# Performance work log

Hardware: AMD Instinct MI355X
Metric: run time of the kernel (lower is better)

## Reference

```python
import jax, jax.numpy as jnp
import numpy as np

T, B, D = 2048, 1, 1024
N_HEAD, D_HEAD, D_FF = 16, 64, 4096
LN_EPS = 1e-5


def layer_norm(x, g, b):
    m = jnp.mean(x, axis=-1, keepdims=True)
    v = jnp.mean(jnp.square(x - m), axis=-1, keepdims=True)
    return (x - m) * jax.lax.rsqrt(v + LN_EPS) * g + b


def rel_shift(x):
    # x: (qlen, klen, bsz, n_head) -> Transformer-XL relative shift
    q, k, b, h = x.shape
    zp = jnp.zeros((q, 1, b, h), dtype=x.dtype)
    x = jnp.concatenate([zp, x], axis=1)            # (q, k+1, b, h)
    x = x.reshape(k + 1, q, b, h)[1:].reshape(q, k, b, h)
    return x


def setup_inputs() -> dict:
    key = jax.random.key(0)
    ks = jax.random.split(key, 12)
    s = lambda fan: 1.0 / np.sqrt(fan)
    inp = {
        "input": jax.random.normal(ks[0], (T, B, D), jnp.float32),
        "pos": jax.random.normal(ks[1], (T, 1, D), jnp.float32),
        "r_w_bias": jax.random.normal(ks[2], (N_HEAD, D_HEAD), jnp.float32) * 0.02,
        "r_r_bias": jax.random.normal(ks[3], (N_HEAD, D_HEAD), jnp.float32) * 0.02,
        # causal mask: True = masked (future positions)
        "mask": jnp.triu(jnp.ones((T, T), dtype=bool), k=1),
        "ln1_g": jnp.ones((D,), jnp.float32),
        "ln1_b": jnp.zeros((D,), jnp.float32),
        "qkv_w": jax.random.normal(ks[4], (D, 3 * D), jnp.float32) * s(D),
        "r_w": jax.random.normal(ks[5], (D, D), jnp.float32) * s(D),
        "o_w": jax.random.normal(ks[6], (D, D), jnp.float32) * s(D),
        "ln2_g": jnp.ones((D,), jnp.float32),
        "ln2_b": jnp.zeros((D,), jnp.float32),
        "ff_w1": jax.random.normal(ks[7], (D, D_FF), jnp.float32) * s(D),
        "ff_b1": jnp.zeros((D_FF,), jnp.float32),
        "ff_w2": jax.random.normal(ks[8], (D_FF, D), jnp.float32) * s(D_FF),
        "ff_b2": jnp.zeros((D,), jnp.float32),
    }
    return inp


def reference(input, pos, r_w_bias, r_r_bias, mask, ln1_g, ln1_b, qkv_w, r_w,
              o_w, ln2_g, ln2_b, ff_w1, ff_b1, ff_w2, ff_b2):
    scale = 1.0 / np.sqrt(D_HEAD)
    # preprocess_attn: layernorm
    q_in = layer_norm(input, ln1_g, ln1_b)                      # (T,B,D)
    w_heads = jnp.einsum('tbd,de->tbe', q_in, qkv_w)            # (T,B,3D)
    w_q, w_k, w_v = jnp.split(w_heads, 3, axis=-1)
    w_q = w_q.reshape(T, B, N_HEAD, D_HEAD)
    w_k = w_k.reshape(T, B, N_HEAD, D_HEAD)
    w_v = w_v.reshape(T, B, N_HEAD, D_HEAD)
    r_k = (pos[:, 0] @ r_w).reshape(T, N_HEAD, D_HEAD)          # (T,h,dh)

    AC = jnp.einsum('ibnd,jbnd->ijbn', w_q + r_w_bias, w_k)     # (T,T,B,h)
    BD = rel_shift(jnp.einsum('ibnd,jnd->ijbn', w_q + r_r_bias, r_k))
    score = (AC + BD) * scale
    score = jnp.where(mask[:, :, None, None], jnp.finfo(score.dtype).min, score)
    probs = jax.nn.softmax(score, axis=1)                       # coverage
    attn_vec = jnp.einsum('ijbn,jbnd->ibnd', probs, w_v).reshape(T, B, D)
    attn_out = jnp.einsum('tbd,de->tbe', attn_vec, o_w)
    # postprocess_attn: (dropout=identity) + residual
    x = input + attn_out
    # FFN block: layernorm > linear-relu-linear > residual
    y = layer_norm(x, ln2_g, ln2_b)
    y = jax.nn.relu(jnp.einsum('tbd,df->tbf', y, ff_w1) + ff_b1)
    y = jnp.einsum('tbf,fd->tbd', y, ff_w2) + ff_b2
    x = x + y
    return x, probs
```

## Files before the change

### kernel.cpp

```cpp
#include <hip/hip_runtime.h>
#include <hip/hip_bf16.h>
#include <stdint.h>

using bf16 = __hip_bfloat16;
using short8 = __attribute__((ext_vector_type(8))) short;
using f32x4 = __attribute__((ext_vector_type(4))) float;

#define T_SEQ 2048
#define DMODEL 1024
#define NHEAD 16
#define DHEAD 64
#define DFF 4096

struct __align__(8) bf16x4 { bf16 x, y, z, w; };

__device__ __forceinline__ void async_cp16(const bf16* g, bf16* l) {
  __builtin_amdgcn_global_load_lds(
      (const __attribute__((address_space(1))) uint32_t*)g,
      (__attribute__((address_space(3))) uint32_t*)l, 16, 0, 0);
}

__global__ __launch_bounds__(256) void transpose_cvt(const float* __restrict__ src,
                                                     bf16* __restrict__ dst,
                                                     int R, int C) {
  __shared__ float tile[32][33];
  int bx = blockIdx.x * 32;
  int by = blockIdx.y * 32;
  int tx = threadIdx.x, ty = threadIdx.y;
#pragma unroll
  for (int r = 0; r < 32; r += 8)
    tile[ty + r][tx] = src[(long)(by + ty + r) * C + bx + tx];
  __syncthreads();
#pragma unroll
  for (int r = 0; r < 32; r += 8)
    dst[(long)(bx + ty + r) * R + by + tx] = __float2bfloat16(tile[tx][ty + r]);
}

__global__ __launch_bounds__(256) void cvt_bf16(const float* __restrict__ src,
                                                bf16* __restrict__ dst, int n4) {
  int idx = blockIdx.x * 256 + threadIdx.x;
  if (idx < n4) {
    float4 v = ((const float4*)src)[idx];
    bf16x4 o{__float2bfloat16(v.x), __float2bfloat16(v.y),
             __float2bfloat16(v.z), __float2bfloat16(v.w)};
    ((bf16x4*)dst)[idx] = o;
  }
}

__global__ __launch_bounds__(256) void ln_cvt(const float* __restrict__ x,
                                              const float* __restrict__ g,
                                              const float* __restrict__ b,
                                              bf16* __restrict__ out) {
  int row = blockIdx.x;
  int tid = threadIdx.x;
  float4 v = ((const float4*)(x + (long)row * DMODEL))[tid];
  float s = v.x + v.y + v.z + v.w;
  float s2 = v.x * v.x + v.y * v.y + v.z * v.z + v.w * v.w;
#pragma unroll
  for (int off = 32; off > 0; off >>= 1) {
    s += __shfl_down(s, off);
    s2 += __shfl_down(s2, off);
  }
  __shared__ float ss[4], ss2[4];
  int wave = tid >> 6, lane = tid & 63;
  if (lane == 0) { ss[wave] = s; ss2[wave] = s2; }
  __syncthreads();
  s = ss[0] + ss[1] + ss[2] + ss[3];
  s2 = ss2[0] + ss2[1] + ss2[2] + ss2[3];
  float mean = s * (1.0f / DMODEL);
  float var = s2 * (1.0f / DMODEL) - mean * mean;
  float rstd = rsqrtf(var + 1e-5f);
  float4 gg = ((const float4*)g)[tid];
  float4 bb = ((const float4*)b)[tid];
  bf16x4 o{__float2bfloat16((v.x - mean) * rstd * gg.x + bb.x),
           __float2bfloat16((v.y - mean) * rstd * gg.y + bb.y),
           __float2bfloat16((v.z - mean) * rstd * gg.z + bb.z),
           __float2bfloat16((v.w - mean) * rstd * gg.w + bb.w)};
  ((bf16x4*)(out + (long)row * DMODEL))[tid] = o;
}

template <int BN, class Epi>
__global__ __launch_bounds__(256) void gemm_bt(const bf16* __restrict__ A,
                                               const bf16* __restrict__ Bt,
                                               int M, int N, int K,
                                               long aZstride, long bZstride, Epi epi) {
  constexpr int BM = 128;
  constexpr int BK = 32;
  constexpr int NT = BN / 32;
  __shared__ bf16 As[BM * BK];
  __shared__ bf16 Bs[BN * BK];

  const int bm = blockIdx.y, bn = blockIdx.x, z = blockIdx.z;
  const bf16* Ab = A + (long)z * aZstride;
  const bf16* Bb = Bt + (long)z * bZstride;

  const int tid = threadIdx.x;
  const int lane = tid & 63;
  const int wave = tid >> 6;
  const int wr = wave >> 1;
  const int wc = wave & 1;
  const int kEnd = epi.kmax(bm, bn, K);

  const f32x4 zero4 = {0.f, 0.f, 0.f, 0.f};
  f32x4 acc[4][NT];
#pragma unroll
  for (int mt = 0; mt < 4; ++mt)
#pragma unroll
    for (int nt = 0; nt < NT; ++nt) acc[mt][nt] = zero4;

  const int sr = tid >> 2;
  const int sc = (tid & 3) * 8;
  const bf16* aG0 = Ab + (long)(bm * BM + sr) * K + sc;
  const bf16* aG1 = Ab + (long)(bm * BM + 64 + sr) * K + sc;
  bf16* aL0 = As + tid * 8;
  bf16* aL1 = As + 2048 + tid * 8;
  const bf16* bG0 = Bb + (long)(bn * BN + sr) * K + sc;
  bf16* bL0 = Bs + tid * 8;
  const bf16* bG1 = Bb + (long)(bn * BN + 64 + sr) * K + sc;
  bf16* bL1 = Bs + 2048 + tid * 8;

  const int aRow = wr * 64 + (lane & 15);
  const int bRow = wc * (BN / 2) + (lane & 15);
  const int kq = (lane >> 4) * 8;

  for (int k0 = 0; k0 < kEnd; k0 += BK) {
    __syncthreads();
    async_cp16(aG0, aL0);
    async_cp16(aG1, aL1);
    async_cp16(bG0, bL0);
    if constexpr (BN == 128) async_cp16(bG1, bL1);
    aG0 += BK; aG1 += BK; bG0 += BK;
    if constexpr (BN == 128) bG1 += BK;
    __syncthreads();
    short8 af[4], bfr[NT];
#pragma unroll
    for (int mt = 0; mt < 4; ++mt)
      af[mt] = *(const short8*)(As + (aRow + mt * 16) * BK + kq);
#pragma unroll
    for (int nt = 0; nt < NT; ++nt)
      bfr[nt] = *(const short8*)(Bs + (bRow + nt * 16) * BK + kq);
#pragma unroll
    for (int mt = 0; mt < 4; ++mt)
#pragma unroll
      for (int nt = 0; nt < NT; ++nt)
        acc[mt][nt] = __builtin_amdgcn_mfma_f32_16x16x32_bf16(af[mt], bfr[nt],
                                                              acc[mt][nt], 0, 0, 0);
  }

  const int rBase = (lane >> 4) * 4;
  const int cOff = lane & 15;
#pragma unroll
  for (int mt = 0; mt < 4; ++mt) {
#pragma unroll
    for (int nt = 0; nt < NT; ++nt) {
      int row = bm * BM + wr * 64 + mt * 16 + rBase;
      int col = bn * BN + wc * (BN / 2) + nt * 16 + cOff;
      f32x4 v = acc[mt][nt];
#pragma unroll
      for (int r = 0; r < 4; ++r) epi.store(z, row + r, col, v[r]);
    }
  }
}

struct EpiQKV {
  bf16 *Qh, *Kb, *Vt;
  __device__ int kmax(int, int, int K) const { return K; }
  __device__ void store(int, int row, int col, float v) const {
    int n = (col >> 6) & 15, d = col & 63;
    long hoff = ((long)n * T_SEQ + row) * DHEAD + d;
    if (col < DMODEL) {
      Qh[hoff] = __float2bfloat16(v);
    } else if (col < 2 * DMODEL) {
      Kb[hoff] = __float2bfloat16(v);
    } else {
      Vt[((long)n * DHEAD + d) * T_SEQ + row] = __float2bfloat16(v);
    }
  }
};

struct EpiRk {
  bf16* Rk;
  __device__ int kmax(int, int, int K) const { return K; }
  __device__ void store(int, int row, int col, float v) const {
    int n = col >> 6, d = col & 63;
    Rk[((long)n * T_SEQ + row) * DHEAD + d] = __float2bfloat16(v);
  }
};

struct EpiPV {
  bf16* av;
  __device__ int kmax(int bm, int, int K) const {
    int kl = (bm + 1) * 128;
    return kl < K ? kl : K;
  }
  __device__ void store(int z, int row, int col, float v) const {
    av[(long)row * DMODEL + z * DHEAD + col] = __float2bfloat16(v);
  }
};

struct EpiO {
  float* xws;
  const float* inp;
  __device__ int kmax(int, int, int K) const { return K; }
  __device__ void store(int, int row, int col, float v) const {
    long idx = (long)row * DMODEL + col;
    xws[idx] = v + inp[idx];
  }
};

struct EpiFF1 {
  bf16* h;
  const float* b1;
  __device__ int kmax(int, int, int K) const { return K; }
  __device__ void store(int, int row, int col, float v) const {
    h[(long)row * DFF + col] = __float2bfloat16(fmaxf(v + b1[col], 0.f));
  }
};

struct EpiFF2 {
  float* out;
  const float* b2;
  const float* xws;
  __device__ int kmax(int, int, int K) const { return K; }
  __device__ void store(int, int row, int col, float v) const {
    long idx = (long)row * DMODEL + col;
    out[idx] = v + b2[col] + xws[idx];
  }
};

__global__ __launch_bounds__(256) void bias_k(const bf16* __restrict__ Kb,
                                              const bf16* __restrict__ Rk,
                                              const float* __restrict__ rwb,
                                              const float* __restrict__ rrb,
                                              float* __restrict__ acB,
                                              float* __restrict__ rrbR) {
  int idx = blockIdx.x * 256 + threadIdx.x;
  int n = idx >> 11;
  const short8* kp = (const short8*)(Kb + (long)idx * DHEAD);
  const short8* rp = (const short8*)(Rk + (long)idx * DHEAD);
  float s1 = 0.f, s2 = 0.f;
#pragma unroll
  for (int q8 = 0; q8 < 8; ++q8) {
    short8 kv = kp[q8], rv = rp[q8];
#pragma unroll
    for (int e = 0; e < 8; ++e) {
      float w1 = rwb[n * DHEAD + q8 * 8 + e];
      float w2 = rrb[n * DHEAD + q8 * 8 + e];
      s1 += w1 * __bfloat162float(((const bf16*)&kv)[e]);
      s2 += w2 * __bfloat162float(((const bf16*)&rv)[e]);
    }
  }
  acB[idx] = s1;
  rrbR[idx] = s2;
}

__global__ __launch_bounds__(256) void score_k(const bf16* __restrict__ Qh,
                                               const bf16* __restrict__ Kb,
                                               const bf16* __restrict__ Rk,
                                               const float* __restrict__ acB,
                                               const float* __restrict__ rrbR,
                                               bf16* __restrict__ score) {
  const int bn = blockIdx.x, bm = blockIdx.y, z = blockIdx.z;
  if (bn > bm) return;
  __shared__ char smem[70656];
  bf16* Qs  = (bf16*)smem;
  bf16* Ks  = (bf16*)(smem + 16384);
  bf16* Bnd = (bf16*)(smem + 32768);

  const int tid = threadIdx.x;
  const int lane = tid & 63, wave = tid >> 6;
  const int wr = wave >> 1, wc = wave & 1;
  const int kq = (lane >> 4) * 8;
  const int l15 = lane & 15;
  const int base = 128 * (bn - bm) + T_SEQ - 1 - 128;

  const bf16* Qg = Qh + ((long)z * T_SEQ + bm * 128) * DHEAD;
  const bf16* Kg = Kb + ((long)z * T_SEQ + bn * 128) * DHEAD;
  const bf16* Rg = Rk + (long)z * T_SEQ * DHEAD;

#pragma unroll
  for (int it = 0; it < 4; ++it) {
    int s = it * 256 + tid;
    int kh = s >> 9, r = (s >> 2) & 127, c = (s & 3) * 8;
    async_cp16(Qg + (long)r * DHEAD + kh * 32 + c, Qs + s * 8);
    async_cp16(Kg + (long)r * DHEAD + kh * 32 + c, Ks + s * 8);
  }
#pragma unroll
  for (int it = 0; it < 8; ++it) {
    int s = it * 256 + tid;
    int kh = s >> 10, u = (s >> 2) & 255, c = (s & 3) * 8;
    int g = base + u;
    g = g < 0 ? 0 : (g > T_SEQ - 1 ? T_SEQ - 1 : g);
    async_cp16(Rg + (long)g * DHEAD + kh * 32 + c, Bnd + s * 8);
  }

  const f32x4 zero4 = {0.f, 0.f, 0.f, 0.f};
  f32x4 accA[4][4], accW[4][8];
#pragma unroll
  for (int mt = 0; mt < 4; ++mt) {
#pragma unroll
    for (int nt = 0; nt < 4; ++nt) accA[mt][nt] = zero4;
#pragma unroll
    for (int ut = 0; ut < 8; ++ut) accW[mt][ut] = zero4;
  }

  __syncthreads();
#pragma unroll
  for (int kh = 0; kh < 2; ++kh) {
    short8 qa[4], kf[4], wf[8];
#pragma unroll
    for (int mt = 0; mt < 4; ++mt)
      qa[mt] = *(const short8*)(Qs + kh * 4096 + (wr * 64 + mt * 16 + l15) * 32 + kq);
#pragma unroll
    for (int nt = 0; nt < 4; ++nt)
      kf[nt] = *(const short8*)(Ks + kh * 4096 + (wc * 64 + nt * 16 + l15) * 32 + kq);
#pragma unroll
    for (int ut = 0; ut < 8; ++ut)
      wf[ut] = *(const short8*)(Bnd + kh * 8192 + (wc * 128 + ut * 16 + l15) * 32 + kq);
#pragma unroll
    for (int mt = 0; mt < 4; ++mt) {
#pragma unroll
      for (int nt = 0; nt < 4; ++nt)
        accA[mt][nt] = __builtin_amdgcn_mfma_f32_16x16x32_bf16(qa[mt], kf[nt], accA[mt][nt], 0, 0, 0);
#pragma unroll
      for (int ut = 0; ut < 8; ++ut)
        accW[mt][ut] = __builtin_amdgcn_mfma_f32_16x16x32_bf16(qa[mt], wf[ut], accW[mt][ut], 0, 0, 0);
    }
  }

  float wbias[8];
#pragma unroll
  for (int ut = 0; ut < 8; ++ut) {
    int u = wc * 128 + ut * 16 + l15;
    int g = base + u;
    g = g < 0 ? 0 : (g > T_SEQ - 1 ? T_SEQ - 1 : g);
    wbias[ut] = rrbR[(long)z * T_SEQ + g];
  }
  float abias[4];
#pragma unroll
  for (int nt = 0; nt < 4; ++nt)
    abias[nt] = acB[(long)z * T_SEQ + bn * 128 + wc * 64 + nt * 16 + l15];

  __syncthreads();

  bf16* Wl = (bf16*)smem + wr * (64 * 276);
  const int quad4 = (lane >> 4) * 4;
  const int umin = wr ? 1 : 65;
  const int umax = wr ? 191 : 255;
#pragma unroll
  for (int mt = 0; mt < 4; ++mt) {
#pragma unroll
    for (int ut = 0; ut < 8; ++ut) {
      int ub = wc * 128 + ut * 16;
      if (ub + 15 < umin || ub > umax) continue;
      int lr = mt * 16 + quad4;
      int u = ub + l15;
#pragma unroll
      for (int reg = 0; reg < 4; ++reg)
        Wl[(lr + reg) * 276 + u] = __float2bfloat16(accW[mt][ut][reg] + wbias[ut]);
    }
  }
  __syncthreads();

  bf16* srow = score + (long)z * T_SEQ * T_SEQ;
#pragma unroll
  for (int mt = 0; mt < 4; ++mt) {
#pragma unroll
    for (int nt = 0; nt < 4; ++nt) {
      int lr = mt * 16 + quad4;
      int c = wc * 64 + nt * 16 + l15;
#pragma unroll
      for (int reg = 0; reg < 4; ++reg) {
        int rl = lr + reg;
        int r = wr * 64 + rl;
        int u = c - r + 128;
        float v = accA[mt][nt][reg] + abias[nt] +
                  __bfloat162float(Wl[rl * 276 + u]);
        srow[(long)(bm * 128 + r) * T_SEQ + bn * 128 + c] = __float2bfloat16(v);
      }
    }
  }
}

__global__ __launch_bounds__(1024) void softmax_k(const bf16* __restrict__ S,
                                                  float* __restrict__ probs,
                                                  bf16* __restrict__ pb) {
  constexpr int HS = T_SEQ + 8;
  __shared__ bf16 pl[NHEAD * HS];
  __shared__ float rinv_s[NHEAD];
  const int i = blockIdx.x;
  const int tid = threadIdx.x;
  const int h = tid >> 6, lane = tid & 63;
  const float scale = 0.125f;
  const int nch = (i >> 9) + 1;

  const bf16* row = S + (long)h * T_SEQ * T_SEQ + (long)i * T_SEQ;

  short8 v[4];
  float m = -1e30f;
#pragma unroll
  for (int c = 0; c < 4; ++c) {
    if (c < nch) {
      int j0 = c * 512 + lane * 8;
      v[c] = *(const short8*)(row + j0);
#pragma unroll
      for (int e = 0; e < 8; ++e) {
        float s = (j0 + e <= i) ? __bfloat162float(((const bf16*)&v[c])[e]) * scale : -1e30f;
        m = fmaxf(m, s);
      }
    }
  }
#pragma unroll
  for (int off = 1; off < 64; off <<= 1) m = fmaxf(m, __shfl_xor(m, off));

  float l = 0.f;
#pragma unroll
  for (int c = 0; c < 4; ++c) {
    if (c < nch) {
      int j0 = c * 512 + lane * 8;
      short8 o;
#pragma unroll
      for (int e = 0; e < 8; ++e) {
        float p = 0.f;
        if (j0 + e <= i) {
          p = __expf(__bfloat162float(((const bf16*)&v[c])[e]) * scale - m);
          l += p;
        }
        ((bf16*)&o)[e] = __float2bfloat16(p);
      }
      *(short8*)(pl + h * HS + j0) = o;
    }
  }
#pragma unroll
  for (int off = 1; off < 64; off <<= 1) l += __shfl_xor(l, off);
  if (lane == 0) rinv_s[h] = 1.f / l;
  __syncthreads();

  float* prow = probs + (long)i * T_SEQ * NHEAD;
  const int n0 = (tid & 3) * 4;
  const float rv0 = rinv_s[n0 + 0], rv1 = rinv_s[n0 + 1];
  const float rv2 = rinv_s[n0 + 2], rv3 = rinv_s[n0 + 3];
#pragma unroll
  for (int it = 0; it < 8; ++it) {
    int o = it * 1024 + tid;
    int j = o >> 2;
    float4 f = {0.f, 0.f, 0.f, 0.f};
    if (j <= i) {
      f.x = __bfloat162float(pl[(n0 + 0) * HS + j]) * rv0;
      f.y = __bfloat162float(pl[(n0 + 1) * HS + j]) * rv1;
      f.z = __bfloat162float(pl[(n0 + 2) * HS + j]) * rv2;
      f.w = __bfloat162float(pl[(n0 + 3) * HS + j]) * rv3;
    }
    ((float4*)prow)[o] = f;
  }

  const int kround = ((i >> 7) + 1) << 7;
  bf16* prow_b = pb + (long)h * T_SEQ * T_SEQ + (long)i * T_SEQ;
  const float rinv = rinv_s[h];
  for (int j0 = lane * 8; j0 < kround; j0 += 512) {
    short8 pv = *(const short8*)(pl + h * HS + j0);
    short8 o;
#pragma unroll
    for (int e = 0; e < 8; ++e)
      ((bf16*)&o)[e] = __float2bfloat16(__bfloat162float(((const bf16*)&pv)[e]) * rinv);
    *(short8*)(prow_b + j0) = o;
  }
}

extern "C" void kernel_launch(void* const* d_in, const int* in_sizes, int n_in,
                              void* d_out, int out_size, void* d_ws, size_t ws_size,
                              hipStream_t stream) {
  const float* input = (const float*)d_in[0];
  const float* pos   = (const float*)d_in[1];
  const float* rwb   = (const float*)d_in[2];
  const float* rrb   = (const float*)d_in[3];
  const float* ln1g  = (const float*)d_in[5];
  const float* ln1b  = (const float*)d_in[6];
  const float* qkvw  = (const float*)d_in[7];
  const float* rw    = (const float*)d_in[8];
  const float* ow    = (const float*)d_in[9];
  const float* ln2g  = (const float*)d_in[10];
  const float* ln2b  = (const float*)d_in[11];
  const float* ffw1  = (const float*)d_in[12];
  const float* ffb1  = (const float*)d_in[13];
  const float* ffw2  = (const float*)d_in[14];
  const float* ffb2  = (const float*)d_in[15];
  float* out = (float*)d_out;

  size_t off = 0;
  auto alloc = [&](size_t bytes) -> char* {
    char* p = (char*)d_ws + off;
    off += (bytes + 255) & ~(size_t)255;
    return p;
  };
  bf16* wqkvT = (bf16*)alloc(3072L * 1024 * 2);
  bf16* wrT   = (bf16*)alloc(1024L * 1024 * 2);
  bf16* woT   = (bf16*)alloc(1024L * 1024 * 2);
  bf16* wf1T  = (bf16*)alloc(4096L * 1024 * 2);
  bf16* wf2T  = (bf16*)alloc(1024L * 4096 * 2);
  bf16* qin   = (bf16*)alloc(2048L * 1024 * 2);
  bf16* posb  = (bf16*)alloc(2048L * 1024 * 2);
  bf16* Qh    = (bf16*)alloc(16L * 2048 * 64 * 2);
  bf16* Kb    = (bf16*)alloc(16L * 2048 * 64 * 2);
  bf16* Vt    = (bf16*)alloc(16L * 64 * 2048 * 2);
  bf16* Rk    = (bf16*)alloc(16L * 2048 * 64 * 2);
  float* acB  = (float*)alloc(16L * 2048 * 4);
  float* rrbR = (float*)alloc(16L * 2048 * 4);
  bf16* ACb   = (bf16*)alloc(16L * 2048 * 2048 * 2);
  bf16* pb    = (bf16*)alloc(16L * 2048 * 2048 * 2);
  bf16* av    = (bf16*)alloc(2048L * 1024 * 2);
  float* xws  = (float*)alloc(2048L * 1024 * 4);
  bf16* yb    = (bf16*)alloc(2048L * 1024 * 2);
  bf16* hb    = (bf16*)alloc(2048L * 4096 * 2);

  dim3 tb(32, 8);
  transpose_cvt<<<dim3(3072 / 32, 1024 / 32), tb, 0, stream>>>(qkvw, wqkvT, 1024, 3072);
  transpose_cvt<<<dim3(1024 / 32, 1024 / 32), tb, 0, stream>>>(rw, wrT, 1024, 1024);
  transpose_cvt<<<dim3(1024 / 32, 1024 / 32), tb, 0, stream>>>(ow, woT, 1024, 1024);
  transpose_cvt<<<dim3(4096 / 32, 1024 / 32), tb, 0, stream>>>(ffw1, wf1T, 1024, 4096);
  transpose_cvt<<<dim3(1024 / 32, 4096 / 32), tb, 0, stream>>>(ffw2, wf2T, 4096, 1024);
  cvt_bf16<<<2048, 256, 0, stream>>>(pos, posb, 2048 * 1024 / 4);
  ln_cvt<<<2048, 256, 0, stream>>>(input, ln1g, ln1b, qin);

  {
    EpiQKV e{Qh, Kb, Vt};
    gemm_bt<128, EpiQKV><<<dim3(24, 16, 1), 256, 0, stream>>>(qin, wqkvT, 2048, 3072, 1024, 0, 0, e);
  }
  {
    EpiRk e{Rk};
    gemm_bt<64, EpiRk><<<dim3(16, 16, 1), 256, 0, stream>>>(posb, wrT, 2048, 1024, 1024, 0, 0, e);
  }
  bias_k<<<128, 256, 0, stream>>>(Kb, Rk, rwb, rrb, acB, rrbR);
  score_k<<<dim3(16, 16, 16), 256, 0, stream>>>(Qh, Kb, Rk, acB, rrbR, ACb);
  softmax_k<<<2048, 1024, 0, stream>>>(ACb, out + 2048L * 1024, pb);
  {
    EpiPV e{av};
    gemm_bt<64, EpiPV><<<dim3(1, 16, 16), 256, 0, stream>>>(pb, Vt, 2048, 64, 2048,
                                                            2048L * 2048, 64L * 2048, e);
  }
  {
    EpiO e{xws, input};
    gemm_bt<64, EpiO><<<dim3(16, 16, 1), 256, 0, stream>>>(av, woT, 2048, 1024, 1024, 0, 0, e);
  }
  ln_cvt<<<2048, 256, 0, stream>>>(xws, ln2g, ln2b, yb);
  {
    EpiFF1 e{hb, ffb1};
    gemm_bt<128, EpiFF1><<<dim3(32, 16, 1), 256, 0, stream>>>(yb, wf1T, 2048, 4096, 1024, 0, 0, e);
  }
  {
    EpiFF2 e{out, ffb2, xws};
    gemm_bt<64, EpiFF2><<<dim3(16, 16, 1), 256, 0, stream>>>(hb, wf2T, 2048, 1024, 4096, 0, 0, e);
  }
}
```

Before: 790.1 us.

## Merge weight-conversion launches, skip masked MFMAs, stage score tile for coalesced stores

Folds the five weight transpose-and-convert launches and the pos conversion into a single launch that picks its matrix from the block index. In the score kernel, it skips MFMAs for AC tiles fully above the diagonal on diagonal blocks, and for positional-band tiles that are never read. The score tile is also staged through shared memory so it can be written with 16-byte coalesced stores instead of scattered 2-byte stores. This adds an extra barrier and LDS round-trip, and upper-triangle values on diagonal blocks now hold only bias terms, which the softmax presumably masks.

```diff
diff --git a/kernel.cpp b/kernel.cpp
--- a/kernel.cpp
+++ b/kernel.cpp
@@ -20,13 +20,33 @@
       (__attribute__((address_space(3))) uint32_t*)l, 16, 0, 0);
 }
 
-__global__ __launch_bounds__(256) void transpose_cvt(const float* __restrict__ src,
-                                                     bf16* __restrict__ dst,
-                                                     int R, int C) {
+__global__ __launch_bounds__(256) void transpose_all(
+    const float* __restrict__ s0, bf16* __restrict__ d0,
+    const float* __restrict__ s1, bf16* __restrict__ d1,
+    const float* __restrict__ s2, bf16* __restrict__ d2,
+    const float* __restrict__ s3, bf16* __restrict__ d3,
+    const float* __restrict__ s4, bf16* __restrict__ d4,
+    const float* __restrict__ s5, bf16* __restrict__ d5) {
   __shared__ float tile[32][33];
-  int bx = blockIdx.x * 32;
-  int by = blockIdx.y * 32;
+  int b = blockIdx.x;
   int tx = threadIdx.x, ty = threadIdx.y;
+  if (b >= 13312) {
+    int idx = (b - 13312) * 256 + ty * 32 + tx;
+    float4 v = ((const float4*)s5)[idx];
+    bf16x4 o{__float2bfloat16(v.x), __float2bfloat16(v.y),
+             __float2bfloat16(v.z), __float2bfloat16(v.w)};
+    ((bf16x4*)d5)[idx] = o;
+    return;
+  }
+  const float* src; bf16* dst; int R, C, t;
+  if (b < 3072)      { src = s0; dst = d0; R = 1024; C = 3072; t = b; }
+  else if (b < 4096) { src = s1; dst = d1; R = 1024; C = 1024; t = b - 3072; }
+  else if (b < 5120) { src = s2; dst = d2; R = 1024; C = 1024; t = b - 4096; }
+  else if (b < 9216) { src = s3; dst = d3; R = 1024; C = 4096; t = b - 5120; }
+  else               { src = s4; dst = d4; R = 4096; C = 1024; t = b - 9216; }
+  int tcols = C >> 5;
+  int bx = (t % tcols) * 32;
+  int by = (t / tcols) * 32;
 #pragma unroll
   for (int r = 0; r < 32; r += 8)
     tile[ty + r][tx] = src[(long)(by + ty + r) * C + bx + tx];
@@ -34,17 +54,6 @@
 #pragma unroll
   for (int r = 0; r < 32; r += 8)
     dst[(long)(bx + ty + r) * R + by + tx] = __float2bfloat16(tile[tx][ty + r]);
-}
-
-__global__ __launch_bounds__(256) void cvt_bf16(const float* __restrict__ src,
-                                                bf16* __restrict__ dst, int n4) {
-  int idx = blockIdx.x * 256 + threadIdx.x;
-  if (idx < n4) {
-    float4 v = ((const float4*)src)[idx];
-    bf16x4 o{__float2bfloat16(v.x), __float2bfloat16(v.y),
-             __float2bfloat16(v.z), __float2bfloat16(v.w)};
-    ((bf16x4*)dst)[idx] = o;
-  }
 }
 
 __global__ __launch_bounds__(256) void ln_cvt(const float* __restrict__ x,
@@ -294,6 +303,23 @@
     async_cp16(Rg + (long)g * DHEAD + kh * 32 + c, Bnd + s * 8);
   }
 
+  int ubs[8];
+  bool keepP[4][8];
+  bool needUt[8];
+#pragma unroll
+  for (int ut = 0; ut < 8; ++ut) { ubs[ut] = (ut * 2 + wc) * 16; needUt[ut] = false; }
+#pragma unroll
+  for (int mt = 0; mt < 4; ++mt) {
+    int r0 = wr * 64 + mt * 16;
+#pragma unroll
+    for (int ut = 0; ut < 8; ++ut) {
+      bool k = (ubs[ut] + 15 >= 113 - r0) && (ubs[ut] <= 255 - r0);
+      keepP[mt][ut] = k;
+      needUt[ut] = needUt[ut] || k;
+    }
+  }
+  const bool diag = (bm == bn);
+
   const f32x4 zero4 = {0.f, 0.f, 0.f, 0.f};
   f32x4 accA[4][4], accW[4][8];
 #pragma unroll
@@ -316,23 +342,25 @@
       kf[nt] = *(const short8*)(Ks + kh * 4096 + (wc * 64 + nt * 16 + l15) * 32 + kq);
 #pragma unroll
     for (int ut = 0; ut < 8; ++ut)
-      wf[ut] = *(const short8*)(Bnd + kh * 8192 + (wc * 128 + ut * 16 + l15) * 32 + kq);
+      if (needUt[ut])
+        wf[ut] = *(const short8*)(Bnd + kh * 8192 + (ubs[ut] + l15) * 32 + kq);
 #pragma unroll
     for (int mt = 0; mt < 4; ++mt) {
 #pragma unroll
       for (int nt = 0; nt < 4; ++nt)
-        accA[mt][nt] = __builtin_amdgcn_mfma_f32_16x16x32_bf16(qa[mt], kf[nt], accA[mt][nt], 0, 0, 0);
+        if (!(diag && (wc * 64 + nt * 16 > wr * 64 + mt * 16 + 15)))
+          accA[mt][nt] = __builtin_amdgcn_mfma_f32_16x16x32_bf16(qa[mt], kf[nt], accA[mt][nt], 0, 0, 0);
 #pragma unroll
       for (int ut = 0; ut < 8; ++ut)
-        accW[mt][ut] = __builtin_amdgcn_mfma_f32_16x16x32_bf16(qa[mt], wf[ut], accW[mt][ut], 0, 0, 0);
+        if (keepP[mt][ut])
+          accW[mt][ut] = __builtin_amdgcn_mfma_f32_16x16x32_bf16(qa[mt], wf[ut], accW[mt][ut], 0, 0, 0);
     }
   }
 
   float wbias[8];
 #pragma unroll
   for (int ut = 0; ut < 8; ++ut) {
-    int u = wc * 128 + ut * 16 + l15;
-    int g = base + u;
+    int g = base + ubs[ut] + l15;
     g = g < 0 ? 0 : (g > T_SEQ - 1 ? T_SEQ - 1 : g);
     wbias[ut] = rrbR[(long)z * T_SEQ + g];
   }
@@ -345,16 +373,13 @@
 
   bf16* Wl = (bf16*)smem + wr * (64 * 276);
   const int quad4 = (lane >> 4) * 4;
-  const int umin = wr ? 1 : 65;
-  const int umax = wr ? 191 : 255;
 #pragma unroll
   for (int mt = 0; mt < 4; ++mt) {
 #pragma unroll
     for (int ut = 0; ut < 8; ++ut) {
-      int ub = wc * 128 + ut * 16;
-      if (ub + 15 < umin || ub > umax) continue;
+      if (!keepP[mt][ut]) continue;
       int lr = mt * 16 + quad4;
-      int u = ub + l15;
+      int u = ubs[ut] + l15;
 #pragma unroll
       for (int reg = 0; reg < 4; ++reg)
         Wl[(lr + reg) * 276 + u] = __float2bfloat16(accW[mt][ut][reg] + wbias[ut]);
@@ -362,7 +387,6 @@
   }
   __syncthreads();
 
-  bf16* srow = score + (long)z * T_SEQ * T_SEQ;
 #pragma unroll
   for (int mt = 0; mt < 4; ++mt) {
 #pragma unroll
@@ -372,13 +396,34 @@
 #pragma unroll
       for (int reg = 0; reg < 4; ++reg) {
         int rl = lr + reg;
-        int r = wr * 64 + rl;
-        int u = c - r + 128;
-        float v = accA[mt][nt][reg] + abias[nt] +
-                  __bfloat162float(Wl[rl * 276 + u]);
-        srow[(long)(bm * 128 + r) * T_SEQ + bn * 128 + c] = __float2bfloat16(v);
+        int u = c - (wr * 64 + rl) + 128;
+        accA[mt][nt][reg] += abias[nt] + __bfloat162float(Wl[rl * 276 + u]);
       }
     }
+  }
+  __syncthreads();
+
+  bf16* Ss = (bf16*)smem;
+#pragma unroll
+  for (int mt = 0; mt < 4; ++mt) {
+#pragma unroll
+    for (int nt = 0; nt < 4; ++nt) {
+      int lr = mt * 16 + quad4;
+      int c = wc * 64 + nt * 16 + l15;
+#pragma unroll
+      for (int reg = 0; reg < 4; ++reg)
+        Ss[(wr * 64 + lr + reg) * 132 + c] = __float2bfloat16(accA[mt][nt][reg]);
+    }
+  }
+  __syncthreads();
+
+  bf16* srow = score + (long)z * T_SEQ * T_SEQ;
+#pragma unroll
+  for (int it = 0; it < 8; ++it) {
+    int s = it * 256 + tid;
+    int row = s >> 4, c8 = (s & 15) * 8;
+    *(short8*)(srow + (long)(bm * 128 + row) * T_SEQ + bn * 128 + c8) =
+        *(const short8*)(Ss + row * 132 + c8);
   }
 }
 
@@ -514,12 +559,8 @@
   bf16* hb    = (bf16*)alloc(2048L * 4096 * 2);
 
   dim3 tb(32, 8);
-  transpose_cvt<<<dim3(3072 / 32, 1024 / 32), tb, 0, stream>>>(qkvw, wqkvT, 1024, 3072);
-  transpose_cvt<<<dim3(1024 / 32, 1024 / 32), tb, 0, stream>>>(rw, wrT, 1024, 1024);
-  transpose_cvt<<<dim3(1024 / 32, 1024 / 32), tb, 0, stream>>>(ow, woT, 1024, 1024);
-  transpose_cvt<<<dim3(4096 / 32, 1024 / 32), tb, 0, stream>>>(ffw1, wf1T, 1024, 4096);
-  transpose_cvt<<<dim3(1024 / 32, 4096 / 32), tb, 0, stream>>>(ffw2, wf2T, 4096, 1024);
-  cvt_bf16<<<2048, 256, 0, stream>>>(pos, posb, 2048 * 1024 / 4);
+  transpose_all<<<15360, tb, 0, stream>>>(qkvw, wqkvT, rw, wrT, ow, woT,
+                                          ffw1, wf1T, ffw2, wf2T, pos, posb);
   ln_cvt<<<2048, 256, 0, stream>>>(input, ln1g, ln1b, qin);
 
   {
```

Measured after the change: 824.6 us. 4.4% more time.

## Merge weight conversions, shrink GEMM tiles, split-K FF2 with atomics

Applied to the files above, without the earlier changes.

Merges the five weight transposes and the pos conversion into one kernel launch. Adds a BM template parameter so the Rk, PV and O GEMMs use 64x64 tiles, doubling their block counts to fill more CUs. FF2 is split four ways along K and accumulates with atomic adds into an output pre-initialised with residual plus bias, which gives more parallelism. The trade-off is extra atomic traffic, non-deterministic summation order and one added init pass.

```diff
diff --git a/kernel.cpp b/kernel.cpp
--- a/kernel.cpp
+++ b/kernel.cpp
@@ -20,13 +20,33 @@
       (__attribute__((address_space(3))) uint32_t*)l, 16, 0, 0);
 }
 
-__global__ __launch_bounds__(256) void transpose_cvt(const float* __restrict__ src,
-                                                     bf16* __restrict__ dst,
-                                                     int R, int C) {
+__global__ __launch_bounds__(256) void transpose_all(
+    const float* __restrict__ s0, bf16* __restrict__ d0,
+    const float* __restrict__ s1, bf16* __restrict__ d1,
+    const float* __restrict__ s2, bf16* __restrict__ d2,
+    const float* __restrict__ s3, bf16* __restrict__ d3,
+    const float* __restrict__ s4, bf16* __restrict__ d4,
+    const float* __restrict__ s5, bf16* __restrict__ d5) {
   __shared__ float tile[32][33];
-  int bx = blockIdx.x * 32;
-  int by = blockIdx.y * 32;
+  int b = blockIdx.x;
   int tx = threadIdx.x, ty = threadIdx.y;
+  if (b >= 13312) {
+    int idx = (b - 13312) * 256 + ty * 32 + tx;
+    float4 v = ((const float4*)s5)[idx];
+    bf16x4 o{__float2bfloat16(v.x), __float2bfloat16(v.y),
+             __float2bfloat16(v.z), __float2bfloat16(v.w)};
+    ((bf16x4*)d5)[idx] = o;
+    return;
+  }
+  const float* src; bf16* dst; int R, C, t;
+  if (b < 3072)      { src = s0; dst = d0; R = 1024; C = 3072; t = b; }
+  else if (b < 4096) { src = s1; dst = d1; R = 1024; C = 1024; t = b - 3072; }
+  else if (b < 5120) { src = s2; dst = d2; R = 1024; C = 1024; t = b - 4096; }
+  else if (b < 9216) { src = s3; dst = d3; R = 1024; C = 4096; t = b - 5120; }
+  else               { src = s4; dst = d4; R = 4096; C = 1024; t = b - 9216; }
+  int tcols = C >> 5;
+  int bx = (t % tcols) * 32;
+  int by = (t / tcols) * 32;
 #pragma unroll
   for (int r = 0; r < 32; r += 8)
     tile[ty + r][tx] = src[(long)(by + ty + r) * C + bx + tx];
@@ -34,17 +54,6 @@
 #pragma unroll
   for (int r = 0; r < 32; r += 8)
     dst[(long)(bx + ty + r) * R + by + tx] = __float2bfloat16(tile[tx][ty + r]);
-}
-
-__global__ __launch_bounds__(256) void cvt_bf16(const float* __restrict__ src,
-                                                bf16* __restrict__ dst, int n4) {
-  int idx = blockIdx.x * 256 + threadIdx.x;
-  if (idx < n4) {
-    float4 v = ((const float4*)src)[idx];
-    bf16x4 o{__float2bfloat16(v.x), __float2bfloat16(v.y),
-             __float2bfloat16(v.z), __float2bfloat16(v.w)};
-    ((bf16x4*)dst)[idx] = o;
-  }
 }
 
 __global__ __launch_bounds__(256) void ln_cvt(const float* __restrict__ x,
@@ -79,13 +88,23 @@
   ((bf16x4*)(out + (long)row * DMODEL))[tid] = o;
 }
 
-template <int BN, class Epi>
+__global__ __launch_bounds__(256) void ff2_init(const float* __restrict__ xws,
+                                                const float* __restrict__ b2,
+                                                float* __restrict__ out) {
+  int idx = blockIdx.x * 256 + threadIdx.x;
+  float4 x = ((const float4*)xws)[idx];
+  float4 b = ((const float4*)b2)[idx & 255];
+  float4 o{x.x + b.x, x.y + b.y, x.z + b.z, x.w + b.w};
+  ((float4*)out)[idx] = o;
+}
+
+template <int BM, int BN, class Epi>
 __global__ __launch_bounds__(256) void gemm_bt(const bf16* __restrict__ A,
                                                const bf16* __restrict__ Bt,
                                                int M, int N, int K,
                                                long aZstride, long bZstride, Epi epi) {
-  constexpr int BM = 128;
   constexpr int BK = 32;
+  constexpr int MT = BM / 32;
   constexpr int NT = BN / 32;
   __shared__ bf16 As[BM * BK];
   __shared__ bf16 Bs[BN * BK];
@@ -99,48 +118,50 @@
   const int wave = tid >> 6;
   const int wr = wave >> 1;
   const int wc = wave & 1;
-  const int kEnd = epi.kmax(bm, bn, K);
+  const int kBeg = epi.kmin(bm, bn, z);
+  const int kEnd = epi.kmax(bm, bn, z, K);
 
   const f32x4 zero4 = {0.f, 0.f, 0.f, 0.f};
-  f32x4 acc[4][NT];
-#pragma unroll
-  for (int mt = 0; mt < 4; ++mt)
+  f32x4 acc[MT][NT];
+#pragma unroll
+  for (int mt = 0; mt < MT; ++mt)
 #pragma unroll
     for (int nt = 0; nt < NT; ++nt) acc[mt][nt] = zero4;
 
   const int sr = tid >> 2;
   const int sc = (tid & 3) * 8;
-  const bf16* aG0 = Ab + (long)(bm * BM + sr) * K + sc;
-  const bf16* aG1 = Ab + (long)(bm * BM + 64 + sr) * K + sc;
+  const bf16* aG0 = Ab + (long)(bm * BM + sr) * K + kBeg + sc;
+  const bf16* aG1 = Ab + (long)(bm * BM + 64 + sr) * K + kBeg + sc;
   bf16* aL0 = As + tid * 8;
   bf16* aL1 = As + 2048 + tid * 8;
-  const bf16* bG0 = Bb + (long)(bn * BN + sr) * K + sc;
+  const bf16* bG0 = Bb + (long)(bn * BN + sr) * K + kBeg + sc;
   bf16* bL0 = Bs + tid * 8;
-  const bf16* bG1 = Bb + (long)(bn * BN + 64 + sr) * K + sc;
+  const bf16* bG1 = Bb + (long)(bn * BN + 64 + sr) * K + kBeg + sc;
   bf16* bL1 = Bs + 2048 + tid * 8;
 
-  const int aRow = wr * 64 + (lane & 15);
+  const int aRow = wr * (BM / 2) + (lane & 15);
   const int bRow = wc * (BN / 2) + (lane & 15);
   const int kq = (lane >> 4) * 8;
 
-  for (int k0 = 0; k0 < kEnd; k0 += BK) {
+  for (int k0 = kBeg; k0 < kEnd; k0 += BK) {
     __syncthreads();
     async_cp16(aG0, aL0);
-    async_cp16(aG1, aL1);
+    if constexpr (BM == 128) async_cp16(aG1, aL1);
     async_cp16(bG0, bL0);
     if constexpr (BN == 128) async_cp16(bG1, bL1);
-    aG0 += BK; aG1 += BK; bG0 += BK;
+    aG0 += BK; bG0 += BK;
+    if constexpr (BM == 128) aG1 += BK;
     if constexpr (BN == 128) bG1 += BK;
     __syncthreads();
-    short8 af[4], bfr[NT];
-#pragma unroll
-    for (int mt = 0; mt < 4; ++mt)
+    short8 af[MT], bfr[NT];
+#pragma unroll
+    for (int mt = 0; mt < MT; ++mt)
       af[mt] = *(const short8*)(As + (aRow + mt * 16) * BK + kq);
 #pragma unroll
     for (int nt = 0; nt < NT; ++nt)
       bfr[nt] = *(const short8*)(Bs + (bRow + nt * 16) * BK + kq);
 #pragma unroll
-    for (int mt = 0; mt < 4; ++mt)
+    for (int mt = 0; mt < MT; ++mt)
 #pragma unroll
       for (int nt = 0; nt < NT; ++nt)
         acc[mt][nt] = __builtin_amdgcn_mfma_f32_16x16x32_bf16(af[mt], bfr[nt],
@@ -150,10 +171,10 @@
   const int rBase = (lane >> 4) * 4;
   const int cOff = lane & 15;
 #pragma unroll
-  for (int mt = 0; mt < 4; ++mt) {
+  for (int mt = 0; mt < MT; ++mt) {
 #pragma unroll
     for (int nt = 0; nt < NT; ++nt) {
-      int row = bm * BM + wr * 64 + mt * 16 + rBase;
+      int row = bm * BM + wr * (BM / 2) + mt * 16 + rBase;
       int col = bn * BN + wc * (BN / 2) + nt * 16 + cOff;
       f32x4 v = acc[mt][nt];
 #pragma unroll
@@ -164,7 +185,8 @@
 
 struct EpiQKV {
   bf16 *Qh, *Kb, *Vt;
-  __device__ int kmax(int, int, int K) const { return K; }
+  __device__ int kmin(int, int, int) const { return 0; }
+  __device__ int kmax(int, int, int, int K) const { return K; }
   __device__ void store(int, int row, int col, float v) const {
     int n = (col >> 6) & 15, d = col & 63;
     long hoff = ((long)n * T_SEQ + row) * DHEAD + d;
@@ -180,7 +202,8 @@
 
 struct EpiRk {
   bf16* Rk;
-  __device__ int kmax(int, int, int K) const { return K; }
+  __device__ int kmin(int, int, int) const { return 0; }
+  __device__ int kmax(int, int, int, int K) const { return K; }
   __device__ void store(int, int row, int col, float v) const {
     int n = col >> 6, d = col & 63;
     Rk[((long)n * T_SEQ + row) * DHEAD + d] = __float2bfloat16(v);
@@ -189,8 +212,9 @@
 
 struct EpiPV {
   bf16* av;
-  __device__ int kmax(int bm, int, int K) const {
-    int kl = (bm + 1) * 128;
+  __device__ int kmin(int, int, int) const { return 0; }
+  __device__ int kmax(int bm, int, int, int K) const {
+    int kl = ((bm >> 1) + 1) * 128;
     return kl < K ? kl : K;
   }
   __device__ void store(int z, int row, int col, float v) const {
@@ -201,7 +225,8 @@
 struct EpiO {
   float* xws;
   const float* inp;
-  __device__ int kmax(int, int, int K) const { return K; }
+  __device__ int kmin(int, int, int) const { return 0; }
+  __device__ int kmax(int, int, int, int K) const { return K; }
   __device__ void store(int, int row, int col, float v) const {
     long idx = (long)row * DMODEL + col;
     xws[idx] = v + inp[idx];
@@ -211,7 +236,8 @@
 struct EpiFF1 {
   bf16* h;
   const float* b1;
-  __device__ int kmax(int, int, int K) const { return K; }
+  __device__ int kmin(int, int, int) const { return 0; }
+  __device__ int kmax(int, int, int, int K) const { return K; }
   __device__ void store(int, int row, int col, float v) const {
     h[(long)row * DFF + col] = __float2bfloat16(fmaxf(v + b1[col], 0.f));
   }
@@ -219,12 +245,13 @@
 
 struct EpiFF2 {
   float* out;
-  const float* b2;
-  const float* xws;
-  __device__ int kmax(int, int, int K) const { return K; }
+  __device__ int kmin(int, int, int z) const { return z * 1024; }
+  __device__ int kmax(int, int, int z, int K) const {
+    int e = z * 1024 + 1024;
+    return e < K ? e : K;
+  }
   __device__ void store(int, int row, int col, float v) const {
-    long idx = (long)row * DMODEL + col;
-    out[idx] = v + b2[col] + xws[idx];
+    unsafeAtomicAdd(&out[(long)row * DMODEL + col], v);
   }
 };
 
@@ -514,41 +541,38 @@
   bf16* hb    = (bf16*)alloc(2048L * 4096 * 2);
 
   dim3 tb(32, 8);
-  transpose_cvt<<<dim3(3072 / 32, 1024 / 32), tb, 0, stream>>>(qkvw, wqkvT, 1024, 3072);
-  transpose_cvt<<<dim3(1024 / 32, 1024 / 32), tb, 0, stream>>>(rw, wrT, 1024, 1024);
-  transpose_cvt<<<dim3(1024 / 32, 1024 / 32), tb, 0, stream>>>(ow, woT, 1024, 1024);
-  transpose_cvt<<<dim3(4096 / 32, 1024 / 32), tb, 0, stream>>>(ffw1, wf1T, 1024, 4096);
-  transpose_cvt<<<dim3(1024 / 32, 4096 / 32), tb, 0, stream>>>(ffw2, wf2T, 4096, 1024);
-  cvt_bf16<<<2048, 256, 0, stream>>>(pos, posb, 2048 * 1024 / 4);
+  transpose_all<<<15360, tb, 0, stream>>>(qkvw, wqkvT, rw, wrT, ow, woT,
+                                          ffw1, wf1T, ffw2, wf2T, pos, posb);
   ln_cvt<<<2048, 256, 0, stream>>>(input, ln1g, ln1b, qin);
 
   {
     EpiQKV e{Qh, Kb, Vt};
-    gemm_bt<128, EpiQKV><<<dim3(24, 16, 1), 256, 0, stream>>>(qin, wqkvT, 2048, 3072, 1024, 0, 0, e);
+    gemm_bt<128, 128, EpiQKV><<<dim3(24, 16, 1), 256, 0, stream>>>(qin, wqkvT, 2048, 3072, 1024, 0, 0, e);
   }
   {
     EpiRk e{Rk};
-    gemm_bt<64, EpiRk><<<dim3(16, 16, 1), 256, 0, stream>>>(posb, wrT, 2048, 1024, 1024, 0, 0, e);
+    gemm_bt<64, 64, EpiRk><<<dim3(16, 32, 1), 256, 0, stream>>>(posb, wrT, 2048, 1024, 1024, 0, 0, e);
   }
   bias_k<<<128, 256, 0, stream>>>(Kb, Rk, rwb, rrb, acB, rrbR);
   score_k<<<dim3(16, 16, 16), 256, 0, stream>>>(Qh, Kb, Rk, acB, rrbR, ACb);
   softmax_k<<<2048, 1024, 0, stream>>>(ACb, out + 2048L * 1024, pb);
   {
     EpiPV e{av};
-    gemm_bt<64, EpiPV><<<dim3(1, 16, 16), 256, 0, stream>>>(pb, Vt, 2048, 64, 2048,
-                                                            2048L * 2048, 64L * 2048, e);
+    gemm_bt<64, 64, EpiPV><<<dim3(1, 32, 16), 256, 0, stream>>>(pb, Vt, 2048, 64, 2048,
+                                                                2048L * 2048, 64L * 2048, e);
   }
   {
     EpiO e{xws, input};
-    gemm_bt<64, EpiO><<<dim3(16, 16, 1), 256, 0, stream>>>(av, woT, 2048, 1024, 1024, 0, 0, e);
-  }
+    gemm_bt<64, 64, EpiO><<<dim3(16, 32, 1), 256, 0, stream>>>(av, woT, 2048, 1024, 1024, 0, 0, e);
+  }
+  ff2_init<<<2048, 256, 0, stream>>>(xws, ffb2, out);
   ln_cvt<<<2048, 256, 0, stream>>>(xws, ln2g, ln2b, yb);
   {
     EpiFF1 e{hb, ffb1};
-    gemm_bt<128, EpiFF1><<<dim3(32, 16, 1), 256, 0, stream>>>(yb, wf1T, 2048, 4096, 1024, 0, 0, e);
+    gemm_bt<128, 128, EpiFF1><<<dim3(32, 16, 1), 256, 0, stream>>>(yb, wf1T, 2048, 4096, 1024, 0, 0, e);
   }
   {
-    EpiFF2 e{out, ffb2, xws};
-    gemm_bt<64, EpiFF2><<<dim3(16, 16, 1), 256, 0, stream>>>(hb, wf2T, 2048, 1024, 4096, 0, 0, e);
-  }
-}
+    EpiFF2 e{out};
+    gemm_bt<128, 64, EpiFF2><<<dim3(16, 16, 4), 256, 0, stream>>>(hb, wf2T, 2048, 1024, 4096, 0, 0, e);
+  }
+}
```

After: 733.2 us. 7.2% less time.
